# Kernel optimization log

Hardware: AMD Instinct MI355X
Metric: run time of the kernel (lower is better)

## Reference

```python
import jax, jax.numpy as jnp
import numpy as np

N_NODES = 100000
N_EDGES = 1600000
NEG_SLOPE = 0.2
EPS = 1e-6


def setup_inputs() -> dict:
    key = jax.random.key(0)
    ks = jax.random.split(key, 14)
    s = 0.1  # weight init scale
    return {
        "x": jax.random.normal(ks[0], (N_NODES, 64), jnp.float32),
        "src": jax.random.randint(ks[1], (N_EDGES,), 0, N_NODES, jnp.int32),
        "dst": jax.random.randint(ks[2], (N_EDGES,), 0, N_NODES, jnp.int32),
        "W0": s * jax.random.normal(ks[3], (64, 128), jnp.float32),
        "al0": s * jax.random.normal(ks[4], (4, 32), jnp.float32),
        "ar0": s * jax.random.normal(ks[5], (4, 32), jnp.float32),
        "W1": s * jax.random.normal(ks[6], (128, 128), jnp.float32),
        "al1": s * jax.random.normal(ks[7], (4, 32), jnp.float32),
        "ar1": s * jax.random.normal(ks[8], (4, 32), jnp.float32),
        "resW1": s * jax.random.normal(ks[9], (128, 128), jnp.float32),
        "W2": s * jax.random.normal(ks[10], (128, 32), jnp.float32),
        "al2": s * jax.random.normal(ks[11], (1, 32), jnp.float32),
        "ar2": s * jax.random.normal(ks[12], (1, 32), jnp.float32),
        "resW2": s * jax.random.normal(ks[13], (128, 32), jnp.float32),
    }


def gat_conv(h, src, dst, W, al, ar, resW):
    """DGL-style GATConv. h: [N, Fin]; returns [N, H, D]."""
    H, D = al.shape
    feat = (h @ W).reshape(-1, H, D)                       # [N,H,D]
    el = jnp.sum(feat * al, axis=-1)                       # [N,H]
    er = jnp.sum(feat * ar, axis=-1)                       # [N,H]
    e = jax.nn.leaky_relu(el[src] + er[dst], NEG_SLOPE)    # [E,H]
    # segment softmax over destination nodes
    m = jax.ops.segment_max(e, dst, num_segments=N_NODES)  # [N,H]
    ex = jnp.exp(e - m[dst])                               # [E,H]
    denom = jax.ops.segment_sum(ex, dst, num_segments=N_NODES)
    alpha = ex / denom[dst]                                # [E,H]
    msg = alpha[:, :, None] * feat[src]                    # [E,H,D]
    rst = jax.ops.segment_sum(msg, dst, num_segments=N_NODES)  # [N,H,D]
    if resW is not None:
        rst = rst + (h @ resW).reshape(-1, H, D)
    return rst


def pairnorm_scs(x, scale=1.0):
    # 'PN-SCS' mode: scale-individually then center by original column mean
    col_mean = jnp.mean(x, axis=0)
    rownorm = jnp.sqrt(EPS + jnp.sum(x * x, axis=1, keepdims=True))
    return scale * x / rownorm - col_mean


def reference(x, src, dst, W0, al0, ar0, W1, al1, ar1, resW1, W2, al2, ar2, resW2):
    # layer 0: no residual, activation applied outside
    h = gat_conv(x, src, dst, W0, al0, ar0, None)          # [N,4,32]
    h = jax.nn.elu(h.reshape(h.shape[0], -1))              # [N,128]
    h = pairnorm_scs(h)
    # middle layer: residual + internal ELU (DGL applies activation inside),
    # then the outer loop flattens and applies ELU again
    h = jax.nn.elu(gat_conv(h, src, dst, W1, al1, ar1, resW1))  # [N,4,32]
    h = jax.nn.elu(h.reshape(h.shape[0], -1))              # [N,128]
    h = pairnorm_scs(h)
    # final layer: residual, mean over heads
    h = gat_conv(h, src, dst, W2, al2, ar2, resW2)         # [N,1,32]
    h = jnp.mean(h, axis=1)                                # [N,32]
    # dgl.mean_nodes readout on a single graph -> mean over nodes
    return jnp.mean(h, axis=0)                             # [32]
```

## Files before the change

### kernel.cpp

```cpp
#include <hip/hip_runtime.h>


typedef __attribute__((ext_vector_type(8))) short s8v;
typedef __attribute__((ext_vector_type(4))) float f4v;
typedef __attribute__((ext_vector_type(2))) float f2v;
typedef __attribute__((ext_vector_type(2))) _Float16 h2;
typedef __attribute__((ext_vector_type(4))) _Float16 h4;

__device__ __forceinline__ unsigned short f2bf(float f) {
  unsigned int x = __float_as_uint(f);
  x += 0x7fffu + ((x >> 16) & 1u);
  return (unsigned short)(x >> 16);
}
__device__ __forceinline__ float bf2f(unsigned short u) {
  return __uint_as_float(((unsigned int)u) << 16);
}
__device__ __forceinline__ unsigned short f2h(float f) {
  _Float16 h = (_Float16)f;
  return __builtin_bit_cast(unsigned short, h);
}
__device__ __forceinline__ unsigned char f2fp8(float v) {
  return (unsigned char)(__builtin_amdgcn_cvt_pk_fp8_f32(v, v, 0, false) & 0xff);
}
__device__ __forceinline__ float lrelu(float x) { return fmaxf(x, 0.2f * x); }
__device__ __forceinline__ float elu1(float x) { return x > 0.f ? x : __expf(x) - 1.f; }

__device__ __forceinline__ void pack_one(const float* W, const float* al, const float* ar,
                                         const float* resW, unsigned short* out,
                                         int K, int M, int BF, int H, int RES0, int t) {
  int c = t / K, k = t - c * K;
  float v = 0.f;
  if (c < BF) {
    v = W[k * BF + c];
  } else if (c < BF + H) {
    int h = c - BF;
    float s = 0.f;
    for (int d = 0; d < 32; d++) s += W[k * BF + h * 32 + d] * al[h * 32 + d];
    v = s;
  } else if (c < BF + 2 * H) {
    int h = c - BF - H;
    float s = 0.f;
    for (int d = 0; d < 32; d++) s += W[k * BF + h * 32 + d] * ar[h * 32 + d];
    v = s;
  } else if (c >= RES0) {
    v = resW[k * (M - RES0) + (c - RES0)];
  }
  unsigned short hi = f2bf(v);
  out[c * K + k] = hi;
  out[M * K + c * K + k] = f2bf(v - bf2f(hi));
}

__global__ __launch_bounds__(256) void hist_pack_k(const int* __restrict__ dst,
                                                   int* __restrict__ bhist, int E, int NB, int chunk, int P2B,
                                                   const float* __restrict__ W0, const float* __restrict__ al0,
                                                   const float* __restrict__ ar0,
                                                   const float* __restrict__ W1, const float* __restrict__ al1,
                                                   const float* __restrict__ ar1, const float* __restrict__ resW1,
                                                   const float* __restrict__ W2, const float* __restrict__ al2,
                                                   const float* __restrict__ ar2, const float* __restrict__ resW2,
                                                   unsigned short* __restrict__ w0t, unsigned short* __restrict__ w1t,
                                                   unsigned short* __restrict__ w2t) {
  if ((int)blockIdx.x < P2B) {
    __shared__ int h[512];
    for (int b = threadIdx.x; b < NB; b += 256) h[b] = 0;
    __syncthreads();
    int e0 = blockIdx.x * chunk;
    int e1 = min(E, e0 + chunk);
    int e = e0 + threadIdx.x * 4;
    for (; e + 3 < e1; e += 1024) {
      int4 d4 = *(const int4*)(dst + e);
      atomicAdd(&h[d4.x >> 8], 1);
      atomicAdd(&h[d4.y >> 8], 1);
      atomicAdd(&h[d4.z >> 8], 1);
      atomicAdd(&h[d4.w >> 8], 1);
    }
    for (; e < e1; e++) atomicAdd(&h[dst[e] >> 8], 1);
    __syncthreads();
    for (int b = threadIdx.x; b < NB; b += 256)
      bhist[(size_t)b * P2B + blockIdx.x] = h[b];
  } else {
    const int n0 = 144 * 64, n1 = 272 * 128, n2 = 80 * 128;
    int t = ((int)blockIdx.x - P2B) * 256 + threadIdx.x;
    if (t < n0) {
      pack_one(W0, al0, ar0, nullptr, w0t, 64, 144, 128, 4, 144, t);
    } else if (t < n0 + n1) {
      pack_one(W1, al1, ar1, resW1, w1t, 128, 272, 128, 4, 144, t - n0);
    } else if (t < n0 + n1 + n2) {
      pack_one(W2, al2, ar2, resW2, w2t, 128, 80, 32, 1, 48, t - n0 - n1);
    }
  }
}

__global__ __launch_bounds__(256) void pscan1(int* __restrict__ arr, int* __restrict__ bsum, int Nn) {
  __shared__ int s[256];
  int t = threadIdx.x;
  int base = blockIdx.x * 1024 + t * 4;
  int v0 = (base + 0 < Nn) ? arr[base + 0] : 0;
  int v1 = (base + 1 < Nn) ? arr[base + 1] : 0;
  int v2 = (base + 2 < Nn) ? arr[base + 2] : 0;
  int v3 = (base + 3 < Nn) ? arr[base + 3] : 0;
  s[t] = v0 + v1 + v2 + v3;
  __syncthreads();
  for (int off = 1; off < 256; off <<= 1) {
    int xv = (t >= off) ? s[t - off] : 0;
    __syncthreads();
    s[t] += xv;
    __syncthreads();
  }
  int excl = t ? s[t - 1] : 0;
  if (t == 255) bsum[blockIdx.x] = s[255];
  if (base + 0 < Nn) { arr[base + 0] = excl; excl += v0; }
  if (base + 1 < Nn) { arr[base + 1] = excl; excl += v1; }
  if (base + 2 < Nn) { arr[base + 2] = excl; excl += v2; }
  if (base + 3 < Nn) { arr[base + 3] = excl; }
}

__global__ __launch_bounds__(256) void bscatter_k(const int* __restrict__ src, const int* __restrict__ dst,
                                                  const int* __restrict__ bhist, const int* __restrict__ bsumB,
                                                  unsigned int* __restrict__ ebuf,
                                                  int E, int NB, int chunk, int nbB) {
  __shared__ int pref[256];
  __shared__ int cur[512];
  int t = threadIdx.x;
  pref[t] = (t < nbB) ? bsumB[t] : 0;
  __syncthreads();
  for (int off = 1; off < 256; off <<= 1) {
    int xv = (t >= off) ? pref[t - off] : 0;
    __syncthreads();
    pref[t] += xv;
    __syncthreads();
  }
  for (int b = t; b < NB; b += 256) {
    size_t idx = (size_t)b * gridDim.x + blockIdx.x;
    int sb = (int)(idx >> 10);
    cur[b] = bhist[idx] + (sb ? pref[sb - 1] : 0);
  }
  __syncthreads();
  int e0 = blockIdx.x * chunk;
  int e1 = min(E, e0 + chunk);
  int e = e0 + t * 4;
  for (; e + 3 < e1; e += 1024) {
    int4 d4 = *(const int4*)(dst + e);
    int4 s4 = *(const int4*)(src + e);
    int p0 = atomicAdd(&cur[d4.x >> 8], 1);
    ebuf[p0] = ((unsigned int)s4.x << 8) | (unsigned int)(d4.x & 255);
    int p1 = atomicAdd(&cur[d4.y >> 8], 1);
    ebuf[p1] = ((unsigned int)s4.y << 8) | (unsigned int)(d4.y & 255);
    int p2 = atomicAdd(&cur[d4.z >> 8], 1);
    ebuf[p2] = ((unsigned int)s4.z << 8) | (unsigned int)(d4.z & 255);
    int p3 = atomicAdd(&cur[d4.w >> 8], 1);
    ebuf[p3] = ((unsigned int)s4.w << 8) | (unsigned int)(d4.w & 255);
  }
  for (; e < e1; e++) {
    int d = dst[e];
    int pos = atomicAdd(&cur[d >> 8], 1);
    ebuf[pos] = ((unsigned int)src[e] << 8) | (unsigned int)(d & 255);
  }
}

__global__ __launch_bounds__(256) void fscatter_k(const unsigned int* __restrict__ ebuf,
                                                  const int* __restrict__ bhist, const int* __restrict__ bsumB,
                                                  int* __restrict__ csr_src,
                                                  int* __restrict__ counts, int* __restrict__ rsp,
                                                  int E, int NB, int P2B, int Nn, int nbB) {
  __shared__ int pref[256];
  __shared__ int cnt[256];
  __shared__ int sc[256];
  __shared__ int cur[256];
  int b = blockIdx.x;
  int t = threadIdx.x;
  pref[t] = (t < nbB) ? bsumB[t] : 0;
  cnt[t] = 0;
  __syncthreads();
  for (int off = 1; off < 256; off <<= 1) {
    int xv = (t >= off) ? pref[t - off] : 0;
    __syncthreads();
    pref[t] += xv;
    __syncthreads();
  }
  size_t i1 = (size_t)b * P2B;
  int sb1 = (int)(i1 >> 10);
  int bstart = bhist[i1] + (sb1 ? pref[sb1 - 1] : 0);
  int bend = E;
  if (b + 1 < NB) {
    size_t i2 = (size_t)(b + 1) * P2B;
    int sb2 = (int)(i2 >> 10);
    bend = bhist[i2] + (sb2 ? pref[sb2 - 1] : 0);
  }
  for (int e = bstart + t; e < bend; e += 256)
    atomicAdd(&cnt[ebuf[e] & 255u], 1);
  __syncthreads();
  int v = cnt[t];
  sc[t] = v;
  __syncthreads();
  for (int off = 1; off < 256; off <<= 1) {
    int xv = (t >= off) ? sc[t - off] : 0;
    __syncthreads();
    sc[t] += xv;
    __syncthreads();
  }
  int base = bstart + (t ? sc[t - 1] : 0);
  int node = (b << 8) + t;
  if (node < Nn) { counts[node] = v; rsp[node] = base; }
  cur[t] = base;
  __syncthreads();
  for (int e = bstart + t; e < bend; e += 256) {
    unsigned int sd = ebuf[e];
    int pos = atomicAdd(&cur[sd & 255u], 1);
    csr_src[pos] = (int)(sd >> 8);
  }
}

__global__ __launch_bounds__(256) void cmw_k(const float* __restrict__ colsum,
                                             const unsigned short* __restrict__ wt,
                                             float* __restrict__ cmw, int K, int M, float invN) {
  int c = blockIdx.x * 256 + threadIdx.x;
  if (c >= M) return;
  float s = 0.f;
  for (int k = 0; k < K; k++)
    s += colsum[k] * (bf2f(wt[c * K + k]) + bf2f(wt[(size_t)M * K + c * K + k]));
  cmw[c] = s * invN;
}

template <int K, int M, int R, int BF, int H, int RES0, bool AF32, bool CMW>
__global__ __launch_bounds__(256) void gemm_bf16(const void* __restrict__ Av,
                                                 const unsigned short* __restrict__ Bt,
                                                 const float* __restrict__ cmw,
                                                 unsigned char* __restrict__ feat8,
                                                 float* __restrict__ el, float* __restrict__ er,
                                                 unsigned short* __restrict__ resh, int nRowTiles) {
  constexpr int NT = M / 16;
  constexpr int PLANE = 16 * K * 2;
  constexpr int RS = (K == 128) ? 8 : 7;
  __shared__ unsigned char bbuf[2 * PLANE];
  int t = threadIdx.x;
  int w = t >> 6;
  int lane = t & 63;
  int tile0 = (int)blockIdx.x * (4 * R) + w * R;
  int r = lane & 15, q = lane >> 4;

  s8v afrag[R][K / 32];
  bool valid[R];
#pragma unroll
  for (int rr = 0; rr < R; rr++) {
    valid[rr] = (tile0 + rr) < nRowTiles;
    if (valid[rr]) {
      if constexpr (AF32) {
        const float* arow = (const float*)Av + (size_t)((tile0 + rr) * 16 + r) * K + q * 8;
#pragma unroll
        for (int kk = 0; kk < K / 32; kk++) {
          s8v v;
#pragma unroll
          for (int j = 0; j < 8; j++) v[j] = (short)f2bf(arow[kk * 32 + j]);
          afrag[rr][kk] = v;
        }
      } else {
        const unsigned short* arow = (const unsigned short*)Av + (size_t)((tile0 + rr) * 16 + r) * K + q * 8;
#pragma unroll
        for (int kk = 0; kk < K / 32; kk++) afrag[rr][kk] = *(const s8v*)(arow + kk * 32);
      }
    }
  }

  const unsigned char* gBhi = (const unsigned char*)Bt;
  const unsigned char* gBlo = (const unsigned char*)Bt + (size_t)M * K * 2;

  uint4 rh = {0, 0, 0, 0}, rl = {0, 0, 0, 0};
  if constexpr (K == 128) {
    rh = *(const uint4*)(gBhi + (size_t)0 * PLANE + t * 16);
    rl = *(const uint4*)(gBlo + (size_t)0 * PLANE + t * 16);
  } else {
    if (t < 128) rh = *(const uint4*)(gBhi + t * 16);
    else         rl = *(const uint4*)(gBlo + (t - 128) * 16);
  }

  for (int ct = 0; ct < NT; ct++) {
    if constexpr (K == 128) {
      unsigned x = (unsigned)t * 16;
      unsigned d = x ^ (((x >> RS) & 7u) << 4);
      *(uint4*)(bbuf + d) = rh;
      *(uint4*)(bbuf + PLANE + d) = rl;
    } else {
      if (t < 128) {
        unsigned x = (unsigned)t * 16;
        unsigned d = x ^ (((x >> RS) & 7u) << 4);
        *(uint4*)(bbuf + d) = rh;
      } else {
        unsigned x = (unsigned)(t - 128) * 16;
        unsigned d = x ^ (((x >> RS) & 7u) << 4);
        *(uint4*)(bbuf + PLANE + d) = rl;
      }
    }
    __syncthreads();
    if (ct + 1 < NT) {
      if constexpr (K == 128) {
        rh = *(const uint4*)(gBhi + (size_t)(ct + 1) * PLANE + t * 16);
        rl = *(const uint4*)(gBlo + (size_t)(ct + 1) * PLANE + t * 16);
      } else {
        if (t < 128) rh = *(const uint4*)(gBhi + (size_t)(ct + 1) * PLANE + t * 16);
        else         rl = *(const uint4*)(gBlo + (size_t)(ct + 1) * PLANE + (t - 128) * 16);
      }
    }
    s8v bhi[K / 32], blo[K / 32];
#pragma unroll
    for (int kk = 0; kk < K / 32; kk++) {
      unsigned off = (unsigned)(q * 16 + kk * 64);
      unsigned ad = ((unsigned)r << RS) + (off ^ (((unsigned)(r & 7)) << 4));
      bhi[kk] = *(const s8v*)(bbuf + ad);
      blo[kk] = *(const s8v*)(bbuf + PLANE + ad);
    }
    int col = ct * 16 + r;
    float cmwv = 0.f;
    if constexpr (CMW) cmwv = cmw[col];
#pragma unroll
    for (int rr = 0; rr < R; rr++) {
      if (!valid[rr]) continue;
      f4v acc = {0.f, 0.f, 0.f, 0.f};
#pragma unroll
      for (int kk = 0; kk < K / 32; kk++) {
        acc = __builtin_amdgcn_mfma_f32_16x16x32_bf16(afrag[rr][kk], bhi[kk], acc, 0, 0, 0);
        acc = __builtin_amdgcn_mfma_f32_16x16x32_bf16(afrag[rr][kk], blo[kk], acc, 0, 0, 0);
      }
      int row0 = (tile0 + rr) * 16 + q * 4;
#pragma unroll
      for (int i = 0; i < 4; i++) {
        float v = acc[i] - cmwv;
        size_t row = (size_t)(row0 + i);
        if (col < BF) {
          feat8[row * BF + col] = f2fp8(v);
        } else if (col < BF + H) {
          el[row * H + (col - BF)] = v;
        } else if (col < BF + 2 * H) {
          er[row * H + (col - BF - H)] = v;
        } else if (RES0 < M && col >= RES0) {
          resh[row * (M - RES0) + (col - RES0)] = f2h(v);
        }
      }
    }
    __syncthreads();
  }
}

template <int MODE>
__global__ __launch_bounds__(256) void aggregate4(const unsigned char* __restrict__ feat8,
                                                  const float* __restrict__ el4,
                                                  const float* __restrict__ er4,
                                                  const int* __restrict__ csr_src,
                                                  const int* __restrict__ rsp,
                                                  const int* __restrict__ counts,
                                                  const unsigned short* __restrict__ resh,
                                                  unsigned short* __restrict__ vbf,
                                                  float* __restrict__ rnrm, int Nn) {
  int n = (int)((blockIdx.x * blockDim.x + threadIdx.x) >> 6);
  if (n >= Nn) return;
  int lane = threadIdx.x & 63;
  int start = __builtin_amdgcn_readfirstlane(rsp[n]);
  int deg = __builtin_amdgcn_readfirstlane(counts[n]);
  int chunks = (deg + 15) >> 4;
  int slot = lane >> 2, h = lane & 3;
  float ern = er4[(size_t)n * 4 + h];
  int hl = lane >> 4;
  unsigned dby = (unsigned)lane << 1;
  f2v a01 = {0.f, 0.f};
  float dsum = 0.f;
  const int* csp0 = csr_src + start;
  int sj[16];
#pragma unroll
  for (int j = 0; j < 16; j++) sj[j] = csp0[j];
  float elv = el4[(size_t)csp0[slot] * 4 + h];
  for (int c = 0; c < chunks; c++) {
    float e = elv + ern;
    float exv = (((c << 4) + slot) < deg) ? __expf(fmaxf(e, 0.2f * e)) : 0.f;
    dsum += exv;
    int sjn[16];
    bool more = (c + 1 < chunks);
    if (more) {
      const int* csp1 = csr_src + start + ((c + 1) << 4);
#pragma unroll
      for (int j = 0; j < 16; j++) sjn[j] = csp1[j];
      elv = el4[(size_t)csp1[slot] * 4 + h];
    }
#pragma unroll
    for (int j = 0; j < 16; j++) {
      float aw = __shfl(exv, (j << 2) | hl);
      unsigned short u = *(const unsigned short*)(feat8 + (((unsigned)sj[j] << 7) + dby));
      f2v fv = __builtin_amdgcn_cvt_pk_f32_fp8((int)u, false);
      f2v aw2 = {aw, aw};
      a01 = __builtin_elementwise_fma(fv, aw2, a01);
    }
    if (more) {
#pragma unroll
      for (int j = 0; j < 16; j++) sj[j] = sjn[j];
    }
  }
#pragma unroll
  for (int off = 4; off < 64; off <<= 1) dsum += __shfl_xor(dsum, off);
  float inv = dsum > 0.f ? 1.f / dsum : 0.f;
  float invh = __shfl(inv, hl);
  float v0, v1;
  if (MODE == 1) {
    h2 rr = *(const h2*)(resh + (size_t)n * 128 + lane * 2);
    v0 = elu1(elu1(a01[0] * invh + (float)rr[0]));
    v1 = elu1(elu1(a01[1] * invh + (float)rr[1]));
  } else {
    v0 = elu1(a01[0] * invh);
    v1 = elu1(a01[1] * invh);
  }
  float ss = v0 * v0 + v1 * v1;
#pragma unroll
  for (int off = 1; off < 64; off <<= 1) ss += __shfl_xor(ss, off);
  float rn = sqrtf(1e-6f + ss);
  float ri = 1.f / rn;
  unsigned int pk = (unsigned int)f2bf(v0 * ri) | ((unsigned int)f2bf(v1 * ri) << 16);
  *(unsigned int*)((char*)vbf + ((size_t)n << 8) + (lane << 2)) = pk;
  if (lane == 0) rnrm[n] = rn;
}

__global__ __launch_bounds__(256) void aggregate1(const unsigned char* __restrict__ feat8,
                                                  const float* __restrict__ el1,
                                                  const float* __restrict__ er1,
                                                  const int* __restrict__ csr_src,
                                                  const int* __restrict__ rsp,
                                                  const int* __restrict__ counts,
                                                  const unsigned short* __restrict__ res2h,
                                                  float* __restrict__ out2, int Nn) {
  int n = (int)((blockIdx.x * blockDim.x + threadIdx.x) >> 6);
  if (n >= Nn) return;
  int lane = threadIdx.x & 63;
  int start = __builtin_amdgcn_readfirstlane(rsp[n]);
  int deg = __builtin_amdgcn_readfirstlane(counts[n]);
  int chunks = (deg + 15) >> 4;
  int l16 = lane & 15;
  float ern = er1[n];
  int g = lane >> 3;
  unsigned dofs4 = (unsigned)(lane & 7) << 2;
  f2v acc01 = {0.f, 0.f}, acc23 = {0.f, 0.f};
  float dsum = 0.f;
  int sA = csr_src[start + l16];
  float elv = el1[sA];
  for (int c = 0; c < chunks; c++) {
    const int* csp = csr_src + start + (c << 4);
    float exv = (((c << 4) + l16) < deg) ? __expf(lrelu(elv + ern)) : 0.f;
    dsum += exv;
    int sAc = sA;
    if (c + 1 < chunks) {
      sA = csp[16 + l16];
      elv = el1[sA];
    }
#pragma unroll
    for (int t = 0; t < 2; t++) {
      int j = (t << 3) + g;
      int sj = __shfl(sAc, j);
      float aw = __shfl(exv, j);
      f2v aw2 = {aw, aw};
      unsigned int u = *(const unsigned int*)(feat8 + (((unsigned)sj << 5) + dofs4));
      f2v fa = __builtin_amdgcn_cvt_pk_f32_fp8((int)u, false);
      f2v fb = __builtin_amdgcn_cvt_pk_f32_fp8((int)u, true);
      acc01 = __builtin_elementwise_fma(fa, aw2, acc01);
      acc23 = __builtin_elementwise_fma(fb, aw2, acc23);
    }
  }
#pragma unroll
  for (int off = 1; off < 16; off <<= 1) dsum += __shfl_xor(dsum, off);
  float inv = dsum > 0.f ? 1.f / dsum : 0.f;
#pragma unroll
  for (int off = 8; off < 64; off <<= 1) {
    acc01[0] += __shfl_xor(acc01[0], off);
    acc01[1] += __shfl_xor(acc01[1], off);
    acc23[0] += __shfl_xor(acc23[0], off);
    acc23[1] += __shfl_xor(acc23[1], off);
  }
  if (lane < 8) {
    h4 rr = *(const h4*)(res2h + (size_t)n * 32 + (lane << 2));
    float4 o;
    o.x = acc01[0] * inv + (float)rr[0];
    o.y = acc01[1] * inv + (float)rr[1];
    o.z = acc23[0] * inv + (float)rr[2];
    o.w = acc23[1] * inv + (float)rr[3];
    *(float4*)(out2 + (size_t)n * 32 + (lane << 2)) = o;
  }
}

__global__ __launch_bounds__(256) void colsum_k(const unsigned short* __restrict__ vbf,
                                                const float* __restrict__ rnrm,
                                                float* __restrict__ colsum, int Nn) {
  __shared__ float2 ls[256];
  int tid = threadIdx.x;
  int c2 = tid & 63;
  int rsub = tid >> 6;
  float2 cs = {0.f, 0.f};
  for (int r = blockIdx.x * 4 + rsub; r < Nn; r += gridDim.x * 4) {
    unsigned u = *(const unsigned*)(vbf + (size_t)r * 128 + c2 * 2);
    float rn = rnrm[r];
    cs.x += bf2f((unsigned short)(u & 0xffffu)) * rn;
    cs.y += bf2f((unsigned short)(u >> 16)) * rn;
  }
  ls[tid] = cs;
  __syncthreads();
  if (tid < 64) {
    float2 a = ls[tid], b = ls[tid + 64], c = ls[tid + 128], d = ls[tid + 192];
    atomicAdd(&colsum[2 * tid], a.x + b.x + c.x + d.x);
    atomicAdd(&colsum[2 * tid + 1], a.y + b.y + c.y + d.y);
  }
}

__global__ __launch_bounds__(256) void final_reduce(const float* __restrict__ out2,
                                                    float* __restrict__ outsum, int Nn) {
  __shared__ float ls[32];
  if (threadIdx.x < 32) ls[threadIdx.x] = 0.f;
  __syncthreads();
  int d = threadIdx.x & 31, rl = threadIdx.x >> 5;
  float acc = 0.f;
  for (int n = blockIdx.x * 8 + rl; n < Nn; n += gridDim.x * 8)
    acc += out2[(size_t)n * 32 + d];
  atomicAdd(&ls[d], acc);
  __syncthreads();
  if (threadIdx.x < 32) atomicAdd(&outsum[threadIdx.x], ls[threadIdx.x]);
}

__global__ void finalize_k(const float* __restrict__ outsum, float* __restrict__ out, float invN) {
  int t = threadIdx.x;
  if (t < 32) out[t] = outsum[t] * invN;
}

extern "C" void kernel_launch(void* const* d_in, const int* in_sizes, int n_in,
                              void* d_out, int out_size, void* d_ws, size_t ws_size,
                              hipStream_t stream) {
  const float* x     = (const float*)d_in[0];
  const int*   src   = (const int*)d_in[1];
  const int*   dst   = (const int*)d_in[2];
  const float* W0    = (const float*)d_in[3];
  const float* al0   = (const float*)d_in[4];
  const float* ar0   = (const float*)d_in[5];
  const float* W1    = (const float*)d_in[6];
  const float* al1   = (const float*)d_in[7];
  const float* ar1   = (const float*)d_in[8];
  const float* resW1 = (const float*)d_in[9];
  const float* W2    = (const float*)d_in[10];
  const float* al2   = (const float*)d_in[11];
  const float* ar2   = (const float*)d_in[12];
  const float* resW2 = (const float*)d_in[13];
  const int N = in_sizes[0] / 64;
  const int E = in_sizes[1];
  const float invN = 1.f / (float)N;
  const int Emax = E + 64;
  const int NB = (N + 255) >> 8;
  const int P2B = 512;
  const int chunk = (((E + P2B - 1) / P2B) + 3) & ~3;
  const int segN = NB * P2B;
  const int nbB = (segN + 1023) / 1024;

  char* p = (char*)d_ws;
  auto alloc = [&](size_t bytes) { char* r = p; p += (bytes + 255) & ~(size_t)255; return r; };

  char* zbase = p;
  float* colsumA = (float*)alloc(512);
  float* colsumB = (float*)alloc(512);
  float* outsum  = (float*)alloc(128);
  size_t zbytes = (size_t)(p - zbase);

  int* counts = (int*)alloc((size_t)4 * N);
  int* rsp    = (int*)alloc((size_t)4 * N);
  int* bsumB  = (int*)alloc(1024);
  int* bhist  = (int*)alloc((size_t)4 * segN);
  unsigned int* ebuf = (unsigned int*)alloc((size_t)4 * E);
  int* csr_src = (int*)alloc((size_t)4 * Emax);
  unsigned char*  feat8 = (unsigned char*)alloc((size_t)N * 128);
  unsigned short* vbf   = (unsigned short*)alloc((size_t)2 * N * 128);
  unsigned short* resh  = (unsigned short*)alloc((size_t)2 * N * 128);
  unsigned short* w0t = (unsigned short*)alloc((size_t)2 * 2 * 144 * 64);
  unsigned short* w1t = (unsigned short*)alloc((size_t)2 * 2 * 272 * 128);
  unsigned short* w2t = (unsigned short*)alloc((size_t)2 * 2 * 80 * 128);
  float* el4  = (float*)alloc((size_t)16 * N);
  float* er4  = (float*)alloc((size_t)16 * N);
  float* rnrm = (float*)alloc((size_t)4 * N);
  float* cmw1 = (float*)alloc(4 * 272);
  float* cmw2 = (float*)alloc(4 * 80);
  float* out2 = (float*)alloc((size_t)4 * N * 32);

  hipMemsetAsync(zbase, 0, zbytes, stream);
  hipMemsetAsync(csr_src + E, 0, (size_t)4 * (Emax - E), stream);

  const int packTot = 144 * 64 + 272 * 128 + 80 * 128;
  const int packBlocks = (packTot + 255) / 256;
  hist_pack_k<<<P2B + packBlocks, 256, 0, stream>>>(dst, bhist, E, NB, chunk, P2B,
                                                    W0, al0, ar0, W1, al1, ar1, resW1,
                                                    W2, al2, ar2, resW2, w0t, w1t, w2t);
  pscan1<<<nbB, 256, 0, stream>>>(bhist, bsumB, segN);
  bscatter_k<<<P2B, 256, 0, stream>>>(src, dst, bhist, bsumB, ebuf, E, NB, chunk, nbB);
  fscatter_k<<<NB, 256, 0, stream>>>(ebuf, bhist, bsumB, csr_src, counts, rsp, E, NB, P2B, N, nbB);

  const int rowTiles = N / 16;
  const int gblocks = (rowTiles + 7) / 8;
  const int aggblocks = (N + 3) / 4;

  gemm_bf16<64, 144, 2, 128, 4, 144, true, false><<<gblocks, 256, 0, stream>>>(
      x, w0t, nullptr, feat8, el4, er4, nullptr, rowTiles);
  aggregate4<0><<<aggblocks, 256, 0, stream>>>(feat8, el4, er4, csr_src, rsp, counts, nullptr, vbf, rnrm, N);
  colsum_k<<<512, 256, 0, stream>>>(vbf, rnrm, colsumA, N);
  cmw_k<<<2, 256, 0, stream>>>(colsumA, w1t, cmw1, 128, 272, invN);

  gemm_bf16<128, 272, 2, 128, 4, 144, false, true><<<gblocks, 256, 0, stream>>>(
      vbf, w1t, cmw1, feat8, el4, er4, resh, rowTiles);
  aggregate4<1><<<aggblocks, 256, 0, stream>>>(feat8, el4, er4, csr_src, rsp, counts, resh, vbf, rnrm, N);
  colsum_k<<<512, 256, 0, stream>>>(vbf, rnrm, colsumB, N);
  cmw_k<<<1, 256, 0, stream>>>(colsumB, w2t, cmw2, 128, 80, invN);

  gemm_bf16<128, 80, 2, 32, 1, 48, false, true><<<gblocks, 256, 0, stream>>>(
      vbf, w2t, cmw2, feat8, el4, er4, resh, rowTiles);
  aggregate1<<<aggblocks, 256, 0, stream>>>(feat8, el4, er4, csr_src, rsp, counts, resh, out2, N);
  final_reduce<<<512, 256, 0, stream>>>(out2, outsum, N);
  finalize_k<<<1, 64, 0, stream>>>(outsum, (float*)d_out, invN);
}
```

Measured before the change: 476.6 us.

## Stage GEMM weight tiles via async global-to-LDS loads and prefetch aggregate gathers

The GEMM now stages several column tiles of the weight matrix at a time straight into double-buffered LDS using global_load_lds, with a single barrier per group instead of two per tile. This cuts the register round-trip and the barrier count. Separately, the aggregate4 kernel now prefetches the fp8 feature gathers for the next chunk of edges into registers while it accumulates the current chunk. This hides gather latency at the cost of more registers and possibly lower occupancy.

```diff
diff --git a/kernel.cpp b/kernel.cpp
--- a/kernel.cpp
+++ b/kernel.cpp
@@ -222,7 +222,7 @@
   cmw[c] = s * invN;
 }
 
-template <int K, int M, int R, int BF, int H, int RES0, bool AF32, bool CMW>
+template <int K, int M, int RC, int R, int BF, int H, int RES0, bool AF32, bool CMW>
 __global__ __launch_bounds__(256) void gemm_bf16(const void* __restrict__ Av,
                                                  const unsigned short* __restrict__ Bt,
                                                  const float* __restrict__ cmw,
@@ -230,9 +230,12 @@
                                                  float* __restrict__ el, float* __restrict__ er,
                                                  unsigned short* __restrict__ resh, int nRowTiles) {
   constexpr int NT = M / 16;
-  constexpr int PLANE = 16 * K * 2;
-  constexpr int RS = (K == 128) ? 8 : 7;
-  __shared__ unsigned char bbuf[2 * PLANE];
+  constexpr int ROWB = K * 2;
+  constexpr int PLANE = 16 * ROWB;
+  constexpr int PLANE2 = 2 * PLANE;
+  constexpr int BUFSZ = RC * PLANE2;
+  constexpr int NR = (NT + RC - 1) / RC;
+  __shared__ __attribute__((aligned(16))) unsigned char buf[2 * BUFSZ];
   int t = threadIdx.x;
   int w = t >> 6;
   int lane = t & 63;
@@ -263,81 +266,77 @@
   }
 
   const unsigned char* gBhi = (const unsigned char*)Bt;
-  const unsigned char* gBlo = (const unsigned char*)Bt + (size_t)M * K * 2;
-
-  uint4 rh = {0, 0, 0, 0}, rl = {0, 0, 0, 0};
-  if constexpr (K == 128) {
-    rh = *(const uint4*)(gBhi + (size_t)0 * PLANE + t * 16);
-    rl = *(const uint4*)(gBlo + (size_t)0 * PLANE + t * 16);
-  } else {
-    if (t < 128) rh = *(const uint4*)(gBhi + t * 16);
-    else         rl = *(const uint4*)(gBlo + (t - 128) * 16);
-  }
-
-  for (int ct = 0; ct < NT; ct++) {
-    if constexpr (K == 128) {
-      unsigned x = (unsigned)t * 16;
-      unsigned d = x ^ (((x >> RS) & 7u) << 4);
-      *(uint4*)(bbuf + d) = rh;
-      *(uint4*)(bbuf + PLANE + d) = rl;
-    } else {
-      if (t < 128) {
-        unsigned x = (unsigned)t * 16;
-        unsigned d = x ^ (((x >> RS) & 7u) << 4);
-        *(uint4*)(bbuf + d) = rh;
-      } else {
-        unsigned x = (unsigned)(t - 128) * 16;
-        unsigned d = x ^ (((x >> RS) & 7u) << 4);
-        *(uint4*)(bbuf + PLANE + d) = rl;
+  const unsigned char* gBlo = gBhi + (size_t)M * K * 2;
+
+  auto stage = [&](int rr, int pb) {
+    int c0 = rr * RC;
+    int nc = NT - c0;
+    if (nc > RC) nc = RC;
+    int bytes = nc * PLANE2;
+    for (int off = t * 16; off < bytes; off += 4096) {
+      int ctl = off / PLANE2;
+      int rem = off - ctl * PLANE2;
+      int pl = rem >= PLANE;
+      int prem = pl ? rem - PLANE : rem;
+      int row = prem / ROWB;
+      int colb = prem - row * ROWB;
+      int gcolb = colb ^ ((row & 7) << 4);
+      const unsigned char* g = (pl ? gBlo : gBhi) + (size_t)(c0 + ctl) * PLANE + row * ROWB + gcolb;
+      __builtin_amdgcn_global_load_lds(
+          (const __attribute__((address_space(1))) void*)g,
+          (__attribute__((address_space(3))) void*)(buf + pb * BUFSZ + off),
+          16, 0, 0);
+    }
+  };
+
+  stage(0, 0);
+  for (int rr = 0; rr < NR; rr++) {
+    int pb = rr & 1;
+    __syncthreads();
+    if (rr + 1 < NR) stage(rr + 1, pb ^ 1);
+    int c0 = rr * RC;
+    int ncts = NT - c0;
+    if (ncts > RC) ncts = RC;
+    for (int cl = 0; cl < ncts; cl++) {
+      int ct = c0 + cl;
+      const unsigned char* base = buf + pb * BUFSZ + cl * PLANE2;
+      s8v bhi[K / 32], blo[K / 32];
+#pragma unroll
+      for (int kk = 0; kk < K / 32; kk++) {
+        unsigned off = (unsigned)(q * 16 + kk * 64);
+        unsigned ad = ((unsigned)r * ROWB) + (off ^ (((unsigned)(r & 7)) << 4));
+        bhi[kk] = *(const s8v*)(base + ad);
+        blo[kk] = *(const s8v*)(base + PLANE + ad);
       }
-    }
-    __syncthreads();
-    if (ct + 1 < NT) {
-      if constexpr (K == 128) {
-        rh = *(const uint4*)(gBhi + (size_t)(ct + 1) * PLANE + t * 16);
-        rl = *(const uint4*)(gBlo + (size_t)(ct + 1) * PLANE + t * 16);
-      } else {
-        if (t < 128) rh = *(const uint4*)(gBhi + (size_t)(ct + 1) * PLANE + t * 16);
-        else         rl = *(const uint4*)(gBlo + (size_t)(ct + 1) * PLANE + (t - 128) * 16);
-      }
-    }
-    s8v bhi[K / 32], blo[K / 32];
-#pragma unroll
-    for (int kk = 0; kk < K / 32; kk++) {
-      unsigned off = (unsigned)(q * 16 + kk * 64);
-      unsigned ad = ((unsigned)r << RS) + (off ^ (((unsigned)(r & 7)) << 4));
-      bhi[kk] = *(const s8v*)(bbuf + ad);
-      blo[kk] = *(const s8v*)(bbuf + PLANE + ad);
-    }
-    int col = ct * 16 + r;
-    float cmwv = 0.f;
-    if constexpr (CMW) cmwv = cmw[col];
-#pragma unroll
-    for (int rr = 0; rr < R; rr++) {
-      if (!valid[rr]) continue;
-      f4v acc = {0.f, 0.f, 0.f, 0.f};
-#pragma unroll
-      for (int kk = 0; kk < K / 32; kk++) {
-        acc = __builtin_amdgcn_mfma_f32_16x16x32_bf16(afrag[rr][kk], bhi[kk], acc, 0, 0, 0);
-        acc = __builtin_amdgcn_mfma_f32_16x16x32_bf16(afrag[rr][kk], blo[kk], acc, 0, 0, 0);
-      }
-      int row0 = (tile0 + rr) * 16 + q * 4;
-#pragma unroll
-      for (int i = 0; i < 4; i++) {
-        float v = acc[i] - cmwv;
-        size_t row = (size_t)(row0 + i);
-        if (col < BF) {
-          feat8[row * BF + col] = f2fp8(v);
-        } else if (col < BF + H) {
-          el[row * H + (col - BF)] = v;
-        } else if (col < BF + 2 * H) {
-          er[row * H + (col - BF - H)] = v;
-        } else if (RES0 < M && col >= RES0) {
-          resh[row * (M - RES0) + (col - RES0)] = f2h(v);
+      int col = ct * 16 + r;
+      float cmwv = 0.f;
+      if constexpr (CMW) cmwv = cmw[col];
+#pragma unroll
+      for (int rr2 = 0; rr2 < R; rr2++) {
+        if (!valid[rr2]) continue;
+        f4v acc = {0.f, 0.f, 0.f, 0.f};
+#pragma unroll
+        for (int kk = 0; kk < K / 32; kk++) {
+          acc = __builtin_amdgcn_mfma_f32_16x16x32_bf16(afrag[rr2][kk], bhi[kk], acc, 0, 0, 0);
+          acc = __builtin_amdgcn_mfma_f32_16x16x32_bf16(afrag[rr2][kk], blo[kk], acc, 0, 0, 0);
+        }
+        int row0 = (tile0 + rr2) * 16 + q * 4;
+#pragma unroll
+        for (int i = 0; i < 4; i++) {
+          float v = acc[i] - cmwv;
+          size_t row = (size_t)(row0 + i);
+          if (col < BF) {
+            feat8[row * BF + col] = f2fp8(v);
+          } else if (col < BF + H) {
+            el[row * H + (col - BF)] = v;
+          } else if (col < BF + 2 * H) {
+            er[row * H + (col - BF - H)] = v;
+          } else if (RES0 < M && col >= RES0) {
+            resh[row * (M - RES0) + (col - RES0)] = f2h(v);
+          }
         }
       }
     }
-    __syncthreads();
   }
 }
 
@@ -364,33 +363,42 @@
   f2v a01 = {0.f, 0.f};
   float dsum = 0.f;
   const int* csp0 = csr_src + start;
-  int sj[16];
-#pragma unroll
-  for (int j = 0; j < 16; j++) sj[j] = csp0[j];
   float elv = el4[(size_t)csp0[slot] * 4 + h];
+  unsigned short ucur[16];
+  {
+    int sj0[16];
+#pragma unroll
+    for (int j = 0; j < 16; j++) sj0[j] = csp0[j];
+#pragma unroll
+    for (int j = 0; j < 16; j++)
+      ucur[j] = *(const unsigned short*)(feat8 + (((unsigned)sj0[j] << 7) + dby));
+  }
   for (int c = 0; c < chunks; c++) {
     float e = elv + ern;
     float exv = (((c << 4) + slot) < deg) ? __expf(fmaxf(e, 0.2f * e)) : 0.f;
     dsum += exv;
-    int sjn[16];
+    unsigned short unx[16];
     bool more = (c + 1 < chunks);
     if (more) {
       const int* csp1 = csr_src + start + ((c + 1) << 4);
+      int sjn[16];
 #pragma unroll
       for (int j = 0; j < 16; j++) sjn[j] = csp1[j];
       elv = el4[(size_t)csp1[slot] * 4 + h];
+#pragma unroll
+      for (int j = 0; j < 16; j++)
+        unx[j] = *(const unsigned short*)(feat8 + (((unsigned)sjn[j] << 7) + dby));
     }
 #pragma unroll
     for (int j = 0; j < 16; j++) {
       float aw = __shfl(exv, (j << 2) | hl);
-      unsigned short u = *(const unsigned short*)(feat8 + (((unsigned)sj[j] << 7) + dby));
-      f2v fv = __builtin_amdgcn_cvt_pk_f32_fp8((int)u, false);
+      f2v fv = __builtin_amdgcn_cvt_pk_f32_fp8((int)ucur[j], false);
       f2v aw2 = {aw, aw};
       a01 = __builtin_elementwise_fma(fv, aw2, a01);
     }
     if (more) {
 #pragma unroll
-      for (int j = 0; j < 16; j++) sj[j] = sjn[j];
+      for (int j = 0; j < 16; j++) ucur[j] = unx[j];
     }
   }
 #pragma unroll
@@ -594,19 +602,19 @@
   const int gblocks = (rowTiles + 7) / 8;
   const int aggblocks = (N + 3) / 4;
 
-  gemm_bf16<64, 144, 2, 128, 4, 144, true, false><<<gblocks, 256, 0, stream>>>(
+  gemm_bf16<64, 144, 4, 2, 128, 4, 144, true, false><<<gblocks, 256, 0, stream>>>(
       x, w0t, nullptr, feat8, el4, er4, nullptr, rowTiles);
   aggregate4<0><<<aggblocks, 256, 0, stream>>>(feat8, el4, er4, csr_src, rsp, counts, nullptr, vbf, rnrm, N);
   colsum_k<<<512, 256, 0, stream>>>(vbf, rnrm, colsumA, N);
   cmw_k<<<2, 256, 0, stream>>>(colsumA, w1t, cmw1, 128, 272, invN);
 
-  gemm_bf16<128, 272, 2, 128, 4, 144, false, true><<<gblocks, 256, 0, stream>>>(
+  gemm_bf16<128, 272, 3, 2, 128, 4, 144, false, true><<<gblocks, 256, 0, stream>>>(
       vbf, w1t, cmw1, feat8, el4, er4, resh, rowTiles);
   aggregate4<1><<<aggblocks, 256, 0, stream>>>(feat8, el4, er4, csr_src, rsp, counts, resh, vbf, rnrm, N);
   colsum_k<<<512, 256, 0, stream>>>(vbf, rnrm, colsumB, N);
   cmw_k<<<1, 256, 0, stream>>>(colsumB, w2t, cmw2, 128, 80, invN);
 
-  gemm_bf16<128, 80, 2, 32, 1, 48, false, true><<<gblocks, 256, 0, stream>>>(
+  gemm_bf16<128, 80, 3, 2, 32, 1, 48, false, true><<<gblocks, 256, 0, stream>>>(
       vbf, w2t, cmw2, feat8, el4, er4, resh, rowTiles);
   aggregate1<<<aggblocks, 256, 0, stream>>>(feat8, el4, er4, csr_src, rsp, counts, resh, out2, N);
   final_reduce<<<512, 256, 0, stream>>>(out2, outsum, N);
```

After: 501.9 us. +5.3%, slower.
